# Optimization experiments

Measured on AMD Instinct MI355X. Metric: run time of the kernel, lower is better.

## Reference

```python
import jax, jax.numpy as jnp
import numpy as np

LOG2E = 1.4426950408889634  # log2(e), same constant as the Triton kernel
TEMPERATURE = 0.07
BLK = 1024  # row-block size for blockwise (flash-style) sum-exp accumulation


def setup_inputs() -> dict:
    key = jax.random.key(0)
    k1, k2 = jax.random.split(key)
    B, D = 8192, 512
    return {
        "image_features": jax.random.normal(k1, (B, D), dtype=jnp.float32),
        "text_features": jax.random.normal(k2, (B, D), dtype=jnp.float32),
    }


def reference(image_features, text_features):
    inv_temp = LOG2E / TEMPERATURE  # kernel's inv_temperature (base-2 units)
    # normalized_inputs=False -> L2-normalize along dim=1 (F.normalize)
    Xn = image_features / jnp.linalg.norm(image_features, axis=1, keepdims=True)
    Yn = text_features / jnp.linalg.norm(text_features, axis=1, keepdims=True)
    B = Xn.shape[0]

    # Blockwise accumulation of row/col sums of exp2(S*inv_temp - inv_temp),
    # never materializing the full BxB similarity matrix (mirrors clip_sum_exp_kernel).
    def step(col_sum, x_blk):
        # x_blk: [BLK, D]; E: [BLK, B]
        E = jnp.exp2(x_blk @ Yn.T * inv_temp - inv_temp)
        return col_sum + E.sum(axis=0), E.sum(axis=1)

    col_sum, row_blocks = jax.lax.scan(
        step, jnp.zeros(B, dtype=jnp.float32), Xn.reshape(B // BLK, BLK, -1)
    )
    row_sum = row_blocks.reshape(B)

    # Diagonal (positive-pair) logits, in base-2 units exactly as the source:
    # Sv = <x_i, y_i> * inv_temp - inv_temp
    Sv = jnp.sum(Xn * Yn, axis=-1) * inv_temp - inv_temp
    # Faithful to source: logits = log(exp(Sv)/row_sum) + log(exp(Sv)/col_sum)
    # (note: source uses natural exp on base-2-scaled Sv; log(exp(Sv)/s) == Sv - log(s))
    logits = (Sv - jnp.log(row_sum)) + (Sv - jnp.log(col_sum))
    loss = -jnp.mean(logits) / 2.0
    return loss
```

## Files before the change

kernel.cpp:

```cpp
#include <hip/hip_runtime.h>

#define NB 8192
#define DD 512
#define INV_T 20.609929155556618f

typedef short bf16x8 __attribute__((ext_vector_type(8)));
typedef float f32x4  __attribute__((ext_vector_type(4)));

__device__ static inline unsigned short f2bf(float f) {
  unsigned int u = __float_as_uint(f);
  u += 0x7fff + ((u >> 16) & 1);
  return (unsigned short)(u >> 16);
}

__device__ static inline void async16(const void* lds, const void* g) {
  __builtin_amdgcn_global_load_lds(
      (const __attribute__((address_space(1))) unsigned int*)g,
      (__attribute__((address_space(3))) unsigned int*)lds, 16, 0, 0);
}

__global__ __launch_bounds__(256) void norm_kernel2(
    const float* __restrict__ X, const float* __restrict__ Y,
    unsigned short* __restrict__ Xnb, unsigned short* __restrict__ Ynb,
    float* __restrict__ Sv) {
  const int wv   = threadIdx.x >> 6;
  const int lane = threadIdx.x & 63;
  const int row  = blockIdx.x * 4 + wv;
  const float4* x4 = (const float4*)(X + (size_t)row * DD);
  const float4* y4 = (const float4*)(Y + (size_t)row * DD);
  float4 xa = x4[lane], xb = x4[lane + 64];
  float4 ya = y4[lane], yb = y4[lane + 64];
  float xs[8] = {xa.x, xa.y, xa.z, xa.w, xb.x, xb.y, xb.z, xb.w};
  float ys[8] = {ya.x, ya.y, ya.z, ya.w, yb.x, yb.y, yb.z, yb.w};
  float ssx = 0.f, ssy = 0.f, sxy = 0.f;
#pragma unroll
  for (int k = 0; k < 8; ++k) {
    ssx += xs[k] * xs[k];
    ssy += ys[k] * ys[k];
    sxy += xs[k] * ys[k];
  }
#pragma unroll
  for (int m = 1; m < 64; m <<= 1) {
    ssx += __shfl_xor(ssx, m);
    ssy += __shfl_xor(ssy, m);
    sxy += __shfl_xor(sxy, m);
  }
  const float rnx = 1.0f / sqrtf(ssx);
  const float rny = 1.0f / sqrtf(ssy);
  unsigned short ox[8], oy[8];
#pragma unroll
  for (int k = 0; k < 8; ++k) {
    ox[k] = f2bf(xs[k] * rnx);
    oy[k] = f2bf(ys[k] * rny);
  }
  *(uint2*)(Xnb + (size_t)row * DD + lane * 4)       = *(const uint2*)&ox[0];
  *(uint2*)(Xnb + (size_t)row * DD + 256 + lane * 4) = *(const uint2*)&ox[4];
  *(uint2*)(Ynb + (size_t)row * DD + lane * 4)       = *(const uint2*)&oy[0];
  *(uint2*)(Ynb + (size_t)row * DD + 256 + lane * 4) = *(const uint2*)&oy[4];
  if (lane == 0) Sv[row] = sxy * rnx * rny * INV_T - INV_T;
}


#define STAGE_A(BUF, T) do {                                                   \
  _Pragma("unroll") for (int h_ = 0; h_ < 2; ++h_) {                           \
    async16(sT + (BUF) + h_ * 16384 + wv * 1024,                               \
            Ab + h_ * 131072 + (T) * 128 + g0);                                \
    async16(sT + (BUF) + h_ * 16384 + 8192 + wv * 1024,                        \
            Ab + h_ * 131072 + (T) * 128 + g1);                                \
  } } while (0)

#define STAGE_B(BUF, T) do {                                                   \
  _Pragma("unroll") for (int h_ = 0; h_ < 2; ++h_) {                           \
    async16(sT + (BUF) + 32768 + h_ * 16384 + wv * 1024,                       \
            Bb + h_ * 131072 + (T) * 128 + g0);                                \
    async16(sT + (BUF) + 32768 + h_ * 16384 + 8192 + wv * 1024,                \
            Bb + h_ * 131072 + (T) * 128 + g1);                                \
  } } while (0)

#define READ_A(BUF, MH) do {                                                   \
  _Pragma("unroll") for (int ks_ = 0; ks_ < 2; ++ks_)                          \
  _Pragma("unroll") for (int i_ = 0; i_ < 4; ++i_)                             \
    af[MH][ks_][i_] = *(const bf16x8*)(sT + (BUF) + raB[ks_]                   \
                                       + (MH) * 8192 + i_ * 2048);             \
  } while (0)

#define READ_B(BUF, J0) do {                                                   \
  _Pragma("unroll") for (int ks_ = 0; ks_ < 2; ++ks_)                          \
  _Pragma("unroll") for (int j_ = 0; j_ < 2; ++j_)                             \
    bfr[ks_][(J0) + j_] = *(const bf16x8*)(sT + (BUF) + rbB[ks_]               \
                                           + ((J0) + j_) * 2048);              \
  } while (0)

#define QUAD(MH, NH) do {                                                      \
  __builtin_amdgcn_s_setprio(1);                                               \
  _Pragma("unroll") for (int ks_ = 0; ks_ < 2; ++ks_)                          \
  _Pragma("unroll") for (int i_ = 0; i_ < 4; ++i_)                             \
  _Pragma("unroll") for (int j_ = 0; j_ < 2; ++j_)                             \
    acc[(MH) * 4 + i_][(NH) * 2 + j_] =                                        \
      __builtin_amdgcn_mfma_f32_16x16x32_bf16(                                 \
        af[MH][ks_][i_], bfr[ks_][(NH) * 2 + j_],                              \
        acc[(MH) * 4 + i_][(NH) * 2 + j_], 0, 0, 0);                           \
  __builtin_amdgcn_s_setprio(0);                                               \
  } while (0)

__global__ __launch_bounds__(512, 1) void gemm_kernel(
    const unsigned short* __restrict__ Xnb, const unsigned short* __restrict__ Ynb,
    float* __restrict__ rowp, float* __restrict__ colp) {
  extern __shared__ __align__(16) char sT[];

  const int tid  = threadIdx.x;
  const int wv   = tid >> 6;
  const int lane = tid & 63;
  const int l16  = lane & 15;
  const int lg   = lane >> 4;
  const int wr   = wv >> 2, wc = wv & 3;

  const int bid = blockIdx.x;
  const int xcd = bid & 7;
  const int idx = bid >> 3;
  const int w   = idx & 31;
  const int br  = (idx >> 5) * 8 + (w & 7);
  const int bc  = xcd * 4 + (w >> 3);

  const int Pl0 = tid * 16;
  const int L0  = Pl0 ^ (((Pl0 >> 7) & 7) << 4);
  const int Pl1 = 8192 + tid * 16;
  const int L1  = Pl1 ^ (((Pl1 >> 7) & 7) << 4);
  const int g0  = (L0 >> 7) * 1024 + (L0 & 127);
  const int g1  = (L1 >> 7) * 1024 + (L1 & 127);
  const char* Ab = (const char*)Xnb + (size_t)br * 262144;
  const char* Bb = (const char*)Ynb + (size_t)bc * 262144;

  const int aswz = (l16 & 7) << 4;
  const int raB[2] = { (wr * 128 + l16) * 128 + ((lg * 16)      ^ aswz),
                       (wr * 128 + l16) * 128 + ((lg * 16 + 64) ^ aswz) };
  const int rbB[2] = { 32768 + (wc * 64 + l16) * 128 + ((lg * 16)      ^ aswz),
                       32768 + (wc * 64 + l16) * 128 + ((lg * 16 + 64) ^ aswz) };

  f32x4  acc[8][4] = {};
  bf16x8 af[2][2][4];
  bf16x8 bfr[2][4];

  STAGE_A(0, 0);
  STAGE_B(0, 0);
  STAGE_A((1 << 16), 1);
  STAGE_B((1 << 16), 1);
  asm volatile("s_waitcnt vmcnt(8)" ::: "memory");
  __builtin_amdgcn_s_barrier();
  asm volatile("" ::: "memory");
  READ_A(0, 0);
  READ_B(0, 0);

  for (int t = 0; t < 8; ++t) {
    const int cur   = (t & 1) << 16;
    const int other = cur ^ (1 << 16);
    READ_A(cur, 1);
    READ_B(cur, 2);
    QUAD(0, 0);
    asm volatile("s_waitcnt lgkmcnt(0)" ::: "memory");
    __builtin_amdgcn_s_barrier();
    if (t < 6) STAGE_A(cur, t + 2);
    QUAD(0, 1);
    __builtin_amdgcn_s_barrier();
    if (t < 6) STAGE_B(cur, t + 2);
    QUAD(1, 0);
    __builtin_amdgcn_s_barrier();
    if (t < 6) {
      asm volatile("s_waitcnt vmcnt(8)" ::: "memory");
    } else if (t == 6) {
      asm volatile("s_waitcnt vmcnt(0)" ::: "memory");
    }
    __builtin_amdgcn_s_barrier();
    asm volatile("" ::: "memory");
    if (t < 7) {
      READ_A(other, 0);
      READ_B(other, 0);
    }
    QUAD(1, 1);
    __builtin_amdgcn_s_barrier();
  }

  __syncthreads();
  float* rp = (float*)sT;
  float* cp = (float*)(sT + 4096);
  float cacc[4] = {0.f, 0.f, 0.f, 0.f};
#pragma unroll
  for (int I = 0; I < 8; ++I) {
    float racc[4] = {0.f, 0.f, 0.f, 0.f};
#pragma unroll
    for (int J = 0; J < 4; ++J)
#pragma unroll
      for (int r = 0; r < 4; ++r) {
        const float e = exp2f(fmaf(acc[I][J][r], INV_T, -INV_T));
        racc[r] += e;
        cacc[J] += e;
      }
#pragma unroll
    for (int r = 0; r < 4; ++r) {
      float v = racc[r];
      v += __shfl_xor(v, 1); v += __shfl_xor(v, 2);
      v += __shfl_xor(v, 4); v += __shfl_xor(v, 8);
      if (l16 == 0) rp[wc * 256 + wr * 128 + I * 16 + lg * 4 + r] = v;
    }
  }
#pragma unroll
  for (int J = 0; J < 4; ++J) {
    float v = cacc[J];
    v += __shfl_xor(v, 16); v += __shfl_xor(v, 32);
    if (lg == 0) cp[wr * 256 + wc * 64 + J * 16 + l16] = v;
  }
  __syncthreads();
  if (tid < 256) {
    rowp[(size_t)bc * NB + br * 256 + tid] =
        rp[tid] + rp[256 + tid] + rp[512 + tid] + rp[768 + tid];
  } else {
    const int c = tid - 256;
    colp[(size_t)br * NB + bc * 256 + c] = cp[c] + cp[256 + c];
  }
}

__global__ __launch_bounds__(256) void loss_kernel(
    const float* __restrict__ rowp, const float* __restrict__ colp,
    const float* __restrict__ Sv, float* __restrict__ out) {
  __shared__ float wsum[4];
  const int i = blockIdx.x * 256 + threadIdx.x;
  float rs = 0.f, cs = 0.f;
#pragma unroll 4
  for (int b = 0; b < 32; ++b) {
    rs += rowp[(size_t)b * NB + i];
    cs += colp[(size_t)b * NB + i];
  }
  float v = 2.f * Sv[i] - logf(rs) - logf(cs);
#pragma unroll
  for (int m = 1; m < 64; m <<= 1) v += __shfl_xor(v, m);
  if ((threadIdx.x & 63) == 0) wsum[threadIdx.x >> 6] = v;
  __syncthreads();
  if (threadIdx.x == 0) {
    const float s = wsum[0] + wsum[1] + wsum[2] + wsum[3];
    atomicAdd(out, s * (-1.0f / (2.0f * NB)));
  }
}

extern "C" void kernel_launch(void* const* d_in, const int* in_sizes, int n_in,
                              void* d_out, int out_size, void* d_ws, size_t ws_size,
                              hipStream_t stream) {
  const float* X = (const float*)d_in[0];
  const float* Y = (const float*)d_in[1];
  char* ws = (char*)d_ws;
  unsigned short* Xnb = (unsigned short*)(ws);
  unsigned short* Ynb = (unsigned short*)(ws + 8388608);
  float* Sv   = (float*)(ws + 16777216);
  float* rowp = (float*)(ws + 16777216 + 32768);
  float* colp = (float*)(ws + 16777216 + 32768 + 1048576);
  float* out  = (float*)d_out;

  (void)hipFuncSetAttribute((const void*)gemm_kernel,
                            hipFuncAttributeMaxDynamicSharedMemorySize,
                            131072);

  hipMemsetAsync(d_out, 0, sizeof(float), stream);
  norm_kernel2<<<NB / 4, 256, 0, stream>>>(X, Y, Xnb, Ynb, Sv);
  gemm_kernel<<<1024, 512, 131072, stream>>>(Xnb, Ynb, rowp, colp);
  loss_kernel<<<32, 256, 0, stream>>>(rowp, colp, Sv, out);
}
```

Measured before the change: 162.4 us.

## Reschedule GEMM main loop into four-phase ping-pong with split register fragments

Restructures the bf16 MFMA main loop so A and B fragments are held in separate named register sets (a0/a1, b01/b23), and LDS reads for the next quadrant are interleaved with MFMA work on the current one. Barriers become phase-end lgkmcnt waits with sched_barrier fences, global-to-LDS staging is placed differently, and the vmcnt wait changes accordingly. The loop is also fully unrolled. Separately, the loss kernel is launched with 64 blocks of 128 threads instead of 32 of 256 for more parallelism. The new schedule risks register pressure and stricter ordering constraints.

```diff
diff --git a/kernel.cpp b/kernel.cpp
--- a/kernel.cpp
+++ b/kernel.cpp
@@ -77,30 +77,36 @@
             Bb + h_ * 131072 + (T) * 128 + g1);                                \
   } } while (0)
 
-#define READ_A(BUF, MH) do {                                                   \
+#define READ_A8(DST, BUF, MH) do {                                             \
   _Pragma("unroll") for (int ks_ = 0; ks_ < 2; ++ks_)                          \
   _Pragma("unroll") for (int i_ = 0; i_ < 4; ++i_)                             \
-    af[MH][ks_][i_] = *(const bf16x8*)(sT + (BUF) + raB[ks_]                   \
-                                       + (MH) * 8192 + i_ * 2048);             \
-  } while (0)
-
-#define READ_B(BUF, J0) do {                                                   \
+    DST[ks_][i_] = *(const bf16x8*)(sT + (BUF) + raB[ks_]                      \
+                                    + (MH) * 8192 + i_ * 2048);                \
+  } while (0)
+
+#define READ_B4(DST, BUF, J0) do {                                             \
   _Pragma("unroll") for (int ks_ = 0; ks_ < 2; ++ks_)                          \
   _Pragma("unroll") for (int j_ = 0; j_ < 2; ++j_)                             \
-    bfr[ks_][(J0) + j_] = *(const bf16x8*)(sT + (BUF) + rbB[ks_]               \
-                                           + ((J0) + j_) * 2048);              \
-  } while (0)
-
-#define QUAD(MH, NH) do {                                                      \
+    DST[ks_][j_] = *(const bf16x8*)(sT + (BUF) + rbB[ks_]                      \
+                                    + ((J0) + j_) * 2048);                     \
+  } while (0)
+
+#define QUADX(MH, NH, A_, B_) do {                                             \
   __builtin_amdgcn_s_setprio(1);                                               \
   _Pragma("unroll") for (int ks_ = 0; ks_ < 2; ++ks_)                          \
   _Pragma("unroll") for (int i_ = 0; i_ < 4; ++i_)                             \
   _Pragma("unroll") for (int j_ = 0; j_ < 2; ++j_)                             \
     acc[(MH) * 4 + i_][(NH) * 2 + j_] =                                        \
       __builtin_amdgcn_mfma_f32_16x16x32_bf16(                                 \
-        af[MH][ks_][i_], bfr[ks_][(NH) * 2 + j_],                              \
+        A_[ks_][i_], B_[ks_][j_],                                              \
         acc[(MH) * 4 + i_][(NH) * 2 + j_], 0, 0, 0);                           \
   __builtin_amdgcn_s_setprio(0);                                               \
+  } while (0)
+
+#define PHASE_END_LGKM() do {                                                  \
+  asm volatile("s_waitcnt lgkmcnt(0)" ::: "memory");                           \
+  __builtin_amdgcn_s_barrier();                                                \
+  __builtin_amdgcn_sched_barrier(0);                                           \
   } while (0)
 
 __global__ __launch_bounds__(512, 1) void gemm_kernel(
@@ -138,8 +144,8 @@
                        32768 + (wc * 64 + l16) * 128 + ((lg * 16 + 64) ^ aswz) };
 
   f32x4  acc[8][4] = {};
-  bf16x8 af[2][2][4];
-  bf16x8 bfr[2][4];
+  bf16x8 a0[2][4], a1[2][4];
+  bf16x8 b01[2][2], b23[2][2];
 
   STAGE_A(0, 0);
   STAGE_B(0, 0);
@@ -147,37 +153,32 @@
   STAGE_B((1 << 16), 1);
   asm volatile("s_waitcnt vmcnt(8)" ::: "memory");
   __builtin_amdgcn_s_barrier();
-  asm volatile("" ::: "memory");
-  READ_A(0, 0);
-  READ_B(0, 0);
-
+  __builtin_amdgcn_sched_barrier(0);
+  READ_A8(a0, 0, 0);
+  READ_B4(b01, 0, 0);
+
+#pragma unroll
   for (int t = 0; t < 8; ++t) {
     const int cur   = (t & 1) << 16;
     const int other = cur ^ (1 << 16);
-    READ_A(cur, 1);
-    READ_B(cur, 2);
-    QUAD(0, 0);
+    READ_A8(a1, cur, 1);
+    QUADX(0, 0, a0, b01);
+    PHASE_END_LGKM();
+    READ_B4(b23, cur, 2);
+    if (t < 6) STAGE_A(cur, t + 2);
+    QUADX(1, 0, a1, b01);
     asm volatile("s_waitcnt lgkmcnt(0)" ::: "memory");
+    if (t < 6)       asm volatile("s_waitcnt vmcnt(4)" ::: "memory");
+    else if (t == 6) asm volatile("s_waitcnt vmcnt(0)" ::: "memory");
     __builtin_amdgcn_s_barrier();
-    if (t < 6) STAGE_A(cur, t + 2);
-    QUAD(0, 1);
-    __builtin_amdgcn_s_barrier();
+    __builtin_amdgcn_sched_barrier(0);
+    if (t < 7) READ_B4(b01, other, 0);
     if (t < 6) STAGE_B(cur, t + 2);
-    QUAD(1, 0);
-    __builtin_amdgcn_s_barrier();
-    if (t < 6) {
-      asm volatile("s_waitcnt vmcnt(8)" ::: "memory");
-    } else if (t == 6) {
-      asm volatile("s_waitcnt vmcnt(0)" ::: "memory");
-    }
-    __builtin_amdgcn_s_barrier();
-    asm volatile("" ::: "memory");
-    if (t < 7) {
-      READ_A(other, 0);
-      READ_B(other, 0);
-    }
-    QUAD(1, 1);
-    __builtin_amdgcn_s_barrier();
+    QUADX(0, 1, a0, b23);
+    PHASE_END_LGKM();
+    QUADX(1, 1, a1, b23);
+    if (t < 7) READ_A8(a0, other, 0);
+    PHASE_END_LGKM();
   }
 
   __syncthreads();
@@ -219,11 +220,11 @@
   }
 }
 
-__global__ __launch_bounds__(256) void loss_kernel(
+__global__ __launch_bounds__(128) void loss_kernel(
     const float* __restrict__ rowp, const float* __restrict__ colp,
     const float* __restrict__ Sv, float* __restrict__ out) {
-  __shared__ float wsum[4];
-  const int i = blockIdx.x * 256 + threadIdx.x;
+  __shared__ float wsum[2];
+  const int i = blockIdx.x * 128 + threadIdx.x;
   float rs = 0.f, cs = 0.f;
 #pragma unroll 4
   for (int b = 0; b < 32; ++b) {
@@ -236,8 +237,7 @@
   if ((threadIdx.x & 63) == 0) wsum[threadIdx.x >> 6] = v;
   __syncthreads();
   if (threadIdx.x == 0) {
-    const float s = wsum[0] + wsum[1] + wsum[2] + wsum[3];
-    atomicAdd(out, s * (-1.0f / (2.0f * NB)));
+    atomicAdd(out, (wsum[0] + wsum[1]) * (-1.0f / (2.0f * NB)));
   }
 }
 
@@ -261,5 +261,5 @@
   hipMemsetAsync(d_out, 0, sizeof(float), stream);
   norm_kernel2<<<NB / 4, 256, 0, stream>>>(X, Y, Xnb, Ynb, Sv);
   gemm_kernel<<<1024, 512, 131072, stream>>>(Xnb, Ynb, rowp, colp);
-  loss_kernel<<<32, 256, 0, stream>>>(rowp, colp, Sv, out);
-}
+  loss_kernel<<<64, 128, 0, stream>>>(rowp, colp, Sv, out);
+}
```

Result: slower. 167.1 us (+2.9%).
